# Kernel optimization log

Measured on AMD Instinct MI355X. Metric: run time of the kernel, lower is better.

The kernel has to match this reference:

```python
import jax, jax.numpy as jnp
from jax import lax
import numpy as np

THRESH = 0.5
R = 4  # suppression radius -> (2R+1)^3 max-pool window


def setup_inputs() -> dict:
    key = jax.random.key(0)
    pred_vol = jax.random.uniform(key, (1, 1, 64, 512, 512), dtype=jnp.float32)
    return {"pred_vol": pred_vol}


def reference(pred_vol):
    # Threshold: keep values above thresh, zero otherwise
    pred_thresh = jnp.where(pred_vol > THRESH, pred_vol, jnp.float32(0.0))
    # 3D max-pool, kernel 2R+1, stride 1, padding R (pad with -inf so padding
    k = 2 * R + 1
    conf = lax.reduce_window(
        pred_thresh,
        -jnp.inf,
        lax.max,
        window_dimensions=(1, 1, k, k, k),
        window_strides=(1, 1, 1, 1, 1),
        padding=[(0, 0), (0, 0), (R, R), (R, R), (R, R)],
    )
    # Keep only strict local maxima of the thresholded volume
    conf = jnp.where((conf > 0.0) & (conf == pred_thresh), conf, jnp.float32(0.0))
    return jnp.squeeze(conf)  # [D, H, W]
```

## Files before the change

### kernel.cpp

```cpp
#include <hip/hip_runtime.h>

static constexpr int Dd = 64;
static constexpr int Hh = 512;
static constexpr int Ww = 512;
static constexpr int RAD = 4;
static constexpr float THRESH_V = 0.5f;
static constexpr int W4 = Ww / 4;
static constexpr int PLANE4 = Hh * W4;

static constexpr int TH = 4;
static constexpr int DC = 16;
static constexpr int ROWS = TH + 2 * RAD;
static constexpr int STEPS = DC + 2 * RAD;
static constexpr int NBLK = (Hh / TH) * (Dd / DC);

typedef float nf4 __attribute__((ext_vector_type(4)));

__device__ __forceinline__ float4 f4max(float4 a, float4 b) {
    return make_float4(fmaxf(a.x, b.x), fmaxf(a.y, b.y), fmaxf(a.z, b.z), fmaxf(a.w, b.w));
}
__device__ __forceinline__ int iclamp(int v, int lo, int hi) {
    return v < lo ? lo : (v > hi ? hi : v);
}

#define LDS_BARRIER() asm volatile("s_waitcnt lgkmcnt(0)\n\ts_barrier" ::: "memory")

__global__ __launch_bounds__(512, 2)
void fused_nms_k(const float4* __restrict__ x4, float4* __restrict__ o4) {
    __shared__ float4 buf[2][ROWS * W4];

    const int tid = threadIdx.x;
    const int w4  = tid & (W4 - 1);
    const int hr  = tid >> 7;
    const int b    = blockIdx.x;
    const int band = b & 7;
    const int rest = b >> 3;
    const int ht   = band * 16 + (rest & 15);
    const int dc   = rest >> 4;
    const int h0   = ht * TH;
    const int d0   = dc * DC;

    const int colm = w4 ? w4 - 1 : 0;
    const int colp = (w4 < W4 - 1) ? w4 + 1 : W4 - 1;

    int off[9];
#pragma unroll
    for (int k = 0; k < 3; ++k) {
        int gh = iclamp(h0 - RAD + hr + 4 * k, 0, Hh - 1);
        off[3 * k]     = gh * W4 + colm;
        off[3 * k + 1] = gh * W4 + w4;
        off[3 * k + 2] = gh * W4 + colp;
    }
    const int outrow = (h0 + hr) * W4 + w4;

    float4 R[8];
    float4 L[9];
    {
        const float4* pl = x4 + (size_t)iclamp(d0 - RAD, 0, Dd - 1) * PLANE4;
#pragma unroll
        for (int i = 0; i < 9; ++i) L[i] = pl[off[i]];
    }

    auto body = [&](int t, int slot, int par, bool emit) {
        float4* B = buf[par];
        float4 o0, o1, o2;
        float4* op[3] = {&o0, &o1, &o2};
#pragma unroll
        for (int k = 0; k < 3; ++k) {
            float4 v0 = L[3 * k], v1 = L[3 * k + 1], v2 = L[3 * k + 2];
            float l3 = v0.w, l2 = fmaxf(v0.z, l3), l1 = fmaxf(v0.y, l2), l0 = fmaxf(v0.x, l1);
            float core = fmaxf(fmaxf(v1.x, v1.y), fmaxf(v1.z, v1.w));
            float r8 = v2.x, r9 = fmaxf(r8, v2.y), r10 = fmaxf(r9, v2.z), r11 = fmaxf(r10, v2.w);
            op[k]->x = fmaxf(l0, fmaxf(core, r8));
            op[k]->y = fmaxf(l1, fmaxf(core, r9));
            op[k]->z = fmaxf(l2, fmaxf(core, r10));
            op[k]->w = fmaxf(l3, fmaxf(core, r11));
        }
        float4 cen;
        if (emit) cen = x4[(size_t)(d0 + t - 2 * RAD) * PLANE4 + outrow];
        if (t + 1 < STEPS) {
            const int gd = iclamp(d0 - RAD + t + 1, 0, Dd - 1);
            const float4* pl = x4 + (size_t)gd * PLANE4;
#pragma unroll
            for (int i = 0; i < 9; ++i) L[i] = pl[off[i]];
        }
        B[0 * 512 + tid] = o0;
        B[1 * 512 + tid] = o1;
        B[2 * 512 + tid] = o2;
        LDS_BARRIER();

        const float4* Bb = B + hr * W4 + w4;
        float4 m = Bb[0];
#pragma unroll
        for (int i = 1; i < 9; ++i) m = f4max(m, Bb[i * W4]);

        if (emit) {
            float4 mm = m;
#pragma unroll
            for (int i = 0; i < 8; ++i) mm = f4max(mm, R[i]);
            nf4 q;
            q.x = (cen.x > THRESH_V && cen.x == mm.x) ? cen.x : 0.0f;
            q.y = (cen.y > THRESH_V && cen.y == mm.y) ? cen.y : 0.0f;
            q.z = (cen.z > THRESH_V && cen.z == mm.z) ? cen.z : 0.0f;
            q.w = (cen.w > THRESH_V && cen.w == mm.w) ? cen.w : 0.0f;
            __builtin_nontemporal_store(
                q, (nf4*)&o4[(size_t)(d0 + t - 2 * RAD) * PLANE4 + outrow]);
        }
        R[slot] = m;
    };

#pragma unroll
    for (int t = 0; t < 8; ++t) body(t, t, t & 1, false);
    for (int tb = 8; tb < STEPS; tb += 8) {
#pragma unroll
        for (int j = 0; j < 8; ++j) body(tb + j, j, j & 1, true);
    }
}

extern "C" void kernel_launch(void* const* d_in, const int* in_sizes, int n_in,
                              void* d_out, int out_size, void* d_ws, size_t ws_size,
                              hipStream_t stream) {
    const float4* x4 = (const float4*)d_in[0];
    float4* out4 = (float4*)d_out;
    (void)d_ws; (void)ws_size; (void)in_sizes; (void)n_in; (void)out_size;
    fused_nms_k<<<dim3(NBLK), dim3(512), 0, stream>>>(x4, out4);
}
```

Before: 129.2 us.

## Stage raw input planes into LDS via global_load_lds and reorder H/W max passes

Each depth plane's 12 input rows are now copied straight into double-buffered LDS with global_load_lds, and the next plane is prefetched while the current one is processed. This replaces the per-thread 9 float4 register loads with their redundant neighbour-column reads. The reduction order becomes H-max from the LDS rows first, then a W-max through a small column buffer, with an extra barrier per step. The vmcnt waits are hand-tuned, so their correctness depends on the exact order in which the centre loads and the async LDS loads are issued.

```diff
diff --git a/kernel.cpp b/kernel.cpp
--- a/kernel.cpp
+++ b/kernel.cpp
@@ -23,15 +23,26 @@
     return v < lo ? lo : (v > hi ? hi : v);
 }
 
-#define LDS_BARRIER() asm volatile("s_waitcnt lgkmcnt(0)\n\ts_barrier" ::: "memory")
+#define BAR_VM(N) asm volatile("s_waitcnt vmcnt(" #N ") lgkmcnt(0)\n\ts_barrier" ::: "memory")
+#define BAR_LDS() asm volatile("s_waitcnt lgkmcnt(0)\n\ts_barrier" ::: "memory")
+
+__device__ __forceinline__ void load_lds16(const float4* g, float4* l) {
+    __builtin_amdgcn_global_load_lds(
+        (const __attribute__((address_space(1))) void*)g,
+        (__attribute__((address_space(3))) void*)l, 16, 0, 0);
+}
 
 __global__ __launch_bounds__(512, 2)
 void fused_nms_k(const float4* __restrict__ x4, float4* __restrict__ o4) {
-    __shared__ float4 buf[2][ROWS * W4];
+    __shared__ float4 braw[2][ROWS * W4];
+    __shared__ float4 bcol[TH * W4];
 
-    const int tid = threadIdx.x;
-    const int w4  = tid & (W4 - 1);
-    const int hr  = tid >> 7;
+    const int tid  = threadIdx.x;
+    const int w4   = tid & (W4 - 1);
+    const int hr   = tid >> 7;
+    const int wid  = tid >> 6;
+    const int lane = tid & 63;
+
     const int b    = blockIdx.x;
     const int band = b & 7;
     const int rest = b >> 3;
@@ -42,60 +53,61 @@
 
     const int colm = w4 ? w4 - 1 : 0;
     const int colp = (w4 < W4 - 1) ? w4 + 1 : W4 - 1;
+    const int outrow = (h0 + hr) * W4 + w4;
 
-    int off[9];
+    int goff[3], loff[3];
 #pragma unroll
     for (int k = 0; k < 3; ++k) {
-        int gh = iclamp(h0 - RAD + hr + 4 * k, 0, Hh - 1);
-        off[3 * k]     = gh * W4 + colm;
-        off[3 * k + 1] = gh * W4 + w4;
-        off[3 * k + 2] = gh * W4 + colp;
+        const int s    = wid + 8 * k;
+        const int row  = s >> 1;
+        const int half = s & 1;
+        const int gh   = iclamp(h0 - RAD + row, 0, Hh - 1);
+        goff[k] = gh * W4 + half * 64 + lane;
+        loff[k] = row * W4 + half * 64;
     }
-    const int outrow = (h0 + hr) * W4 + w4;
+
+    auto stage = [&](int t, int par) {
+        const int gd = iclamp(d0 - RAD + t, 0, Dd - 1);
+        const float4* pl = x4 + (size_t)gd * PLANE4;
+#pragma unroll
+        for (int k = 0; k < 3; ++k)
+            load_lds16(pl + goff[k], &braw[par][loff[k]]);
+    };
 
     float4 R[8];
-    float4 L[9];
-    {
-        const float4* pl = x4 + (size_t)iclamp(d0 - RAD, 0, Dd - 1) * PLANE4;
-#pragma unroll
-        for (int i = 0; i < 9; ++i) L[i] = pl[off[i]];
-    }
 
-    auto body = [&](int t, int slot, int par, bool emit) {
-        float4* B = buf[par];
-        float4 o0, o1, o2;
-        float4* op[3] = {&o0, &o1, &o2};
-#pragma unroll
-        for (int k = 0; k < 3; ++k) {
-            float4 v0 = L[3 * k], v1 = L[3 * k + 1], v2 = L[3 * k + 2];
-            float l3 = v0.w, l2 = fmaxf(v0.z, l3), l1 = fmaxf(v0.y, l2), l0 = fmaxf(v0.x, l1);
-            float core = fmaxf(fmaxf(v1.x, v1.y), fmaxf(v1.z, v1.w));
-            float r8 = v2.x, r9 = fmaxf(r8, v2.y), r10 = fmaxf(r9, v2.z), r11 = fmaxf(r10, v2.w);
-            op[k]->x = fmaxf(l0, fmaxf(core, r8));
-            op[k]->y = fmaxf(l1, fmaxf(core, r9));
-            op[k]->z = fmaxf(l2, fmaxf(core, r10));
-            op[k]->w = fmaxf(l3, fmaxf(core, r11));
+    auto body = [&](int t, int slot, int par, bool emit, bool emitPrev) {
+        if (emitPrev) BAR_VM(1); else BAR_VM(0);
+
+        float4 cen;
+        if (emit) {
+            cen = x4[(size_t)(d0 + t - 2 * RAD) * PLANE4 + outrow];
+            __builtin_amdgcn_sched_barrier(0);
         }
-        float4 cen;
-        if (emit) cen = x4[(size_t)(d0 + t - 2 * RAD) * PLANE4 + outrow];
-        if (t + 1 < STEPS) {
-            const int gd = iclamp(d0 - RAD + t + 1, 0, Dd - 1);
-            const float4* pl = x4 + (size_t)gd * PLANE4;
-#pragma unroll
-            for (int i = 0; i < 9; ++i) L[i] = pl[off[i]];
-        }
-        B[0 * 512 + tid] = o0;
-        B[1 * 512 + tid] = o1;
-        B[2 * 512 + tid] = o2;
-        LDS_BARRIER();
+        if (t + 1 < STEPS) stage(t + 1, par ^ 1);
 
-        const float4* Bb = B + hr * W4 + w4;
-        float4 m = Bb[0];
-#pragma unroll
-        for (int i = 1; i < 9; ++i) m = f4max(m, Bb[i * W4]);
+        const float4* Bc = &braw[par][hr * W4 + w4];
+        float4 m = f4max(Bc[0 * W4], Bc[1 * W4]);
+        m = f4max(m, f4max(Bc[2 * W4], Bc[3 * W4]));
+        m = f4max(m, f4max(Bc[4 * W4], Bc[5 * W4]));
+        m = f4max(m, f4max(Bc[6 * W4], Bc[7 * W4]));
+        m = f4max(m, Bc[8 * W4]);
+        bcol[hr * W4 + w4] = m;
+        BAR_LDS();
+
+        const float4 lmv = bcol[hr * W4 + colm];
+        const float4 rmv = bcol[hr * W4 + colp];
+        const float l3 = lmv.w, l2 = fmaxf(lmv.z, l3), l1 = fmaxf(lmv.y, l2), l0 = fmaxf(lmv.x, l1);
+        const float core = fmaxf(fmaxf(m.x, m.y), fmaxf(m.z, m.w));
+        const float r0 = rmv.x, r1 = fmaxf(r0, rmv.y), r2 = fmaxf(r1, rmv.z), r3 = fmaxf(r2, rmv.w);
+        float4 pm;
+        pm.x = fmaxf(l0, fmaxf(core, r0));
+        pm.y = fmaxf(l1, fmaxf(core, r1));
+        pm.z = fmaxf(l2, fmaxf(core, r2));
+        pm.w = fmaxf(l3, fmaxf(core, r3));
 
         if (emit) {
-            float4 mm = m;
+            float4 mm = pm;
 #pragma unroll
             for (int i = 0; i < 8; ++i) mm = f4max(mm, R[i]);
             nf4 q;
@@ -106,15 +118,17 @@
             __builtin_nontemporal_store(
                 q, (nf4*)&o4[(size_t)(d0 + t - 2 * RAD) * PLANE4 + outrow]);
         }
-        R[slot] = m;
+        R[slot] = pm;
     };
 
+    stage(0, 0);
 #pragma unroll
-    for (int t = 0; t < 8; ++t) body(t, t, t & 1, false);
-    for (int tb = 8; tb < STEPS; tb += 8) {
+    for (int t = 0; t < 8; ++t) body(t, t, t & 1, false, false);
+    body(8, 0, 0, true, false);
 #pragma unroll
-        for (int j = 0; j < 8; ++j) body(tb + j, j, j & 1, true);
-    }
+    for (int j = 1; j < 8; ++j) body(8 + j, j, j & 1, true, true);
+#pragma unroll
+    for (int j = 0; j < 8; ++j) body(16 + j, j, j & 1, true, true);
 }
 
 extern "C" void kernel_launch(void* const* d_in, const int* in_sizes, int n_in,
```

Measured after the change: 123.8 us. 4.2% less time.
